# Performance work log

Hardware: AMD Instinct MI355X
Metric: run time of the kernel (lower is better)

The kernel has to match this reference:

```python
import jax, jax.numpy as jnp
import numpy as np

N = 100000   # users
E = 50000    # hyperedges per timestep
NNZ = 800000 # incidences per timestep
T = 8        # step_split
D = 64       # embed_dim


def setup_inputs() -> dict:
    key = jax.random.key(0)
    ks = jax.random.split(key, 9)
    s = 1.0 / np.sqrt(D)
    return {
        "user_emb": jax.random.normal(ks[0], (N, D), jnp.float32) * s,
        "W_conv": jax.random.normal(ks[1], (D, D), jnp.float32) * s,
        "b_conv": jnp.zeros((D,), jnp.float32),
        "fus_w1": jax.random.normal(ks[2], (D, D), jnp.float32) * s,
        "fus_b1": jnp.zeros((D,), jnp.float32),
        "fus_w2": jax.random.normal(ks[3], (D, 1), jnp.float32) * s,
        "fus_b2": jnp.zeros((1,), jnp.float32),
        "edge_nodes": jax.random.randint(ks[4], (T, NNZ), 0, N),
        "edge_hyper": jax.random.randint(ks[5], (T, NNZ), 0, E),
    }


def _hconv(h, nodes, hyper):
    # h: [N, D] transformed node feats; nodes/hyper: [NNZ] incidence list
    ones = jnp.ones((nodes.shape[0], 1), h.dtype)
    e_sum = jax.ops.segment_sum(h[nodes], hyper, num_segments=E)      # [E, D]
    e_cnt = jax.ops.segment_sum(ones, hyper, num_segments=E)          # [E, 1]
    e = e_sum / jnp.maximum(e_cnt, 1.0)
    n_sum = jax.ops.segment_sum(e[hyper], nodes, num_segments=N)      # [N, D]
    n_cnt = jax.ops.segment_sum(ones, nodes, num_segments=N)          # [N, 1]
    return n_sum / jnp.maximum(n_cnt, 1.0)


def _fuse(hidden, dy, w1, b1, w2, b2):
    emb = jnp.stack([hidden, dy], axis=0)                             # [2, N, D]
    score = jax.nn.softmax(jnp.tanh(emb @ w1 + b1) @ w2 + b2, axis=0)  # [2, N, 1]
    return jnp.sum(score * emb, axis=0)                                # [N, D]


def reference(user_emb, W_conv, b_conv, fus_w1, fus_b1, fus_w2, fus_b2,
              edge_nodes, edge_hyper):
    # Conv input is always the raw user embedding table -> per-step convs independent.
    h = jax.nn.relu(user_emb @ W_conv + b_conv)                        # [N, D]
    conv_out = jax.vmap(lambda nd, hy: _hconv(h, nd, hy))(edge_nodes, edge_hyper)  # [T, N, D]

    def step(carry, dy):
        out = _fuse(carry, dy, fus_w1, fus_b1, fus_w2, fus_b2)
        return out, None

    final, _ = jax.lax.scan(step, conv_out[0], conv_out[1:])
    return final
```

## Files before the change

kernel.cpp:

```cpp
#include <hip/hip_runtime.h>
#include <hip/hip_bf16.h>

#define N_USERS 100000
#define E_HYPER 50000
#define NNZ_E   800000
#define T_STEPS 8
#define DIM     64

typedef __bf16 bf16x8 __attribute__((ext_vector_type(8)));
typedef float  f32x4  __attribute__((ext_vector_type(4)));

__device__ __forceinline__ float ld_in(const void* p, size_t i, int f32)
{
    return f32 ? ((const float*)p)[i]
               : __bfloat162float(((const __hip_bfloat16*)p)[i]);
}

__global__ void k_detect(const unsigned short* __restrict__ raw, int* __restrict__ flag)
{
    __shared__ int cnt;
    if (threadIdx.x == 0) cnt = 0;
    __syncthreads();
    int c = 0;
    for (int i = threadIdx.x; i < 4096; i += blockDim.x) {
        int e = (raw[i] >> 7) & 0xFF;
        if (e > 126) c++;
    }
    atomicAdd(&cnt, c);
    __syncthreads();
    if (threadIdx.x == 0) *flag = (cnt > 64) ? 1 : 0;
}

__global__ void k_convert_params(
    const void* W, const void* b, const void* w1, const void* b1,
    const void* w2, const void* b2, const int* __restrict__ flag,
    float* __restrict__ st)
{
    int f = *flag;
    int i = blockIdx.x * blockDim.x + threadIdx.x;
    if (i < 4096)          st[i] = ld_in(W,  i,        f);
    else if (i < 4160)     st[i] = ld_in(b,  i - 4096, f);
    else if (i < 8256)     st[i] = ld_in(w1, i - 4160, f);
    else if (i < 8320)     st[i] = ld_in(b1, i - 8256, f);
    else if (i < 8384)     st[i] = ld_in(w2, i - 8320, f);
    else if (i == 8384)    st[i] = ld_in(b2, 0,        f);
}

__global__ __launch_bounds__(256) void k_transform(
    const void* __restrict__ emb, const int* __restrict__ flag,
    const float* __restrict__ st, __hip_bfloat16* __restrict__ h)
{
    __shared__ float Wl[DIM * DIM];
    __shared__ float bl[DIM];
    for (int i = threadIdx.x; i < DIM * DIM; i += blockDim.x) Wl[i] = st[i];
    if (threadIdx.x < DIM) bl[threadIdx.x] = st[4096 + threadIdx.x];
    __syncthreads();

    int f = *flag;
    int wave = threadIdx.x >> 6, lane = threadIdx.x & 63;
    int wavesTotal = gridDim.x * (blockDim.x >> 6);
    for (int row = blockIdx.x * (blockDim.x >> 6) + wave; row < N_USERS;
         row += wavesTotal) {
        size_t base = (size_t)row * DIM;
        float v = ld_in(emb, base + lane, f);
        float acc = bl[lane];
#pragma unroll
        for (int k = 0; k < DIM; ++k)
            acc += __shfl(v, k, 64) * Wl[k * DIM + lane];
        h[base + lane] = __float2bfloat16(fmaxf(acc, 0.f));
    }
}

__global__ __launch_bounds__(256) void k_build(
    const int* __restrict__ nodes, const int* __restrict__ hyper,
    int* __restrict__ head_e, int* __restrict__ next_e,
    int* __restrict__ head_n, int* __restrict__ next_n)
{
    int i = blockIdx.x * blockDim.x + threadIdx.x;
    if (i >= NNZ_E) return;
    next_e[i] = atomicExch(&head_e[hyper[i]], i);
    next_n[i] = atomicExch(&head_n[nodes[i]], i);
}

__global__ __launch_bounds__(256) void k_gather_e(
    const __hip_bfloat16* __restrict__ h,
    const int* __restrict__ nodes,
    const int* __restrict__ head_e, const int* __restrict__ next_e,
    __hip_bfloat16* __restrict__ e)
{
    int lane = threadIdx.x & 63;
    int wid = blockIdx.x * (blockDim.x >> 6) + (threadIdx.x >> 6);
    int nW  = gridDim.x * (blockDim.x >> 6);
    for (int s0 = wid * 4; s0 < E_HYPER; s0 += nW * 4) {
        int idx[4]; float acc[4]; int cnt[4];
#pragma unroll
        for (int c = 0; c < 4; ++c) {
            int sg = s0 + c;
            idx[c] = (sg < E_HYPER) ? head_e[sg] : -1;
            acc[c] = 0.f; cnt[c] = 0;
        }
        while (idx[0] >= 0 || idx[1] >= 0 || idx[2] >= 0 || idx[3] >= 0) {
            int nxt[4], nd[4];
#pragma unroll
            for (int c = 0; c < 4; ++c)
                if (idx[c] >= 0) { nxt[c] = next_e[idx[c]]; nd[c] = nodes[idx[c]]; }
#pragma unroll
            for (int c = 0; c < 4; ++c)
                if (idx[c] >= 0) {
                    acc[c] += __bfloat162float(h[(size_t)nd[c] * DIM + lane]);
                    cnt[c]++; idx[c] = nxt[c];
                }
        }
#pragma unroll
        for (int c = 0; c < 4; ++c) {
            int sg = s0 + c;
            if (sg < E_HYPER)
                e[(size_t)sg * DIM + lane] =
                    __float2bfloat16(acc[c] / (float)max(cnt[c], 1));
        }
    }
}

__device__ __forceinline__ float ld_carry(void* out, float* cws, size_t i,
                                          int f, int use_ws)
{
    if (f) return ((float*)out)[i];
    if (use_ws) return cws[i];
    return __bfloat162float(((__hip_bfloat16*)out)[i]);
}
__device__ __forceinline__ void st_carry(void* out, float* cws, size_t i,
                                         int f, int use_ws, int wr, float v)
{
    if (f) { ((float*)out)[i] = v; return; }
    if (use_ws) {
        cws[i] = v;
        if (wr) ((__hip_bfloat16*)out)[i] = __float2bfloat16(v);
        return;
    }
    ((__hip_bfloat16*)out)[i] = __float2bfloat16(v);
}

__global__ __launch_bounds__(256) void k_gather_n(
    const __hip_bfloat16* __restrict__ e,
    const int* __restrict__ hyper,
    const int* __restrict__ head_n, const int* __restrict__ next_n,
    float* __restrict__ dy,
    void* __restrict__ out, float* __restrict__ cws,
    const int* __restrict__ flag, int use_ws, int to_carry)
{
    int f = *flag;
    int lane = threadIdx.x & 63;
    int wid = blockIdx.x * (blockDim.x >> 6) + (threadIdx.x >> 6);
    int nW  = gridDim.x * (blockDim.x >> 6);
    for (int s0 = wid * 4; s0 < N_USERS; s0 += nW * 4) {
        int idx[4]; float acc[4]; int cnt[4];
#pragma unroll
        for (int c = 0; c < 4; ++c) {
            int sg = s0 + c;
            idx[c] = (sg < N_USERS) ? head_n[sg] : -1;
            acc[c] = 0.f; cnt[c] = 0;
        }
        while (idx[0] >= 0 || idx[1] >= 0 || idx[2] >= 0 || idx[3] >= 0) {
            int nxt[4], hy[4];
#pragma unroll
            for (int c = 0; c < 4; ++c)
                if (idx[c] >= 0) { nxt[c] = next_n[idx[c]]; hy[c] = hyper[idx[c]]; }
#pragma unroll
            for (int c = 0; c < 4; ++c)
                if (idx[c] >= 0) {
                    acc[c] += __bfloat162float(e[(size_t)hy[c] * DIM + lane]);
                    cnt[c]++; idx[c] = nxt[c];
                }
        }
#pragma unroll
        for (int c = 0; c < 4; ++c) {
            int sg = s0 + c;
            if (sg < N_USERS) {
                float v = acc[c] / (float)max(cnt[c], 1);
                size_t o = (size_t)sg * DIM + lane;
                if (to_carry) st_carry(out, cws, o, f, use_ws, 0, v);
                else          dy[o] = v;
            }
        }
    }
}

__global__ __launch_bounds__(256) void k_fuse_mfma(
    void* __restrict__ dout, float* __restrict__ cws,
    const float* __restrict__ dy_buf,
    const float* __restrict__ st, const int* __restrict__ flag,
    int use_ws, int write_out)
{
    int f = *flag;
    float* cf = f ? (float*)dout : (use_ws ? cws : (float*)0);
    __hip_bfloat16* cb = (__hip_bfloat16*)dout;

    int lane = threadIdx.x & 63;
    int quad = lane >> 4;
    int m    = lane & 15;

    bf16x8 bw[4][2];
    float b1v[4], w2v[4];
#pragma unroll
    for (int nt = 0; nt < 4; ++nt) {
#pragma unroll
        for (int kb = 0; kb < 2; ++kb)
#pragma unroll
            for (int j = 0; j < 8; ++j) {
                int k = kb * 32 + quad * 8 + j;
                bw[nt][kb][j] = (__bf16)st[4160 + k * 64 + nt * 16 + m];
            }
        b1v[nt] = st[8256 + nt * 16 + m];
        w2v[nt] = st[8320 + nt * 16 + m];
    }

    int wid = blockIdx.x * (blockDim.x >> 6) + (threadIdx.x >> 6);
    int nW  = gridDim.x * (blockDim.x >> 6);
    const int NT = N_USERS / 16;

    for (int tile = wid; tile < NT; tile += nW) {
        int row = tile * 16 + m;
        size_t base = (size_t)row * DIM;

        float hidf[2][8], dyf[2][8];
        if (cf) {
            const f32x4* cp = (const f32x4*)(cf + base);
            const f32x4* dp = (const f32x4*)(dy_buf + base);
#pragma unroll
            for (int kb = 0; kb < 2; ++kb) {
                f32x4 a = cp[kb * 8 + quad * 2], b = cp[kb * 8 + quad * 2 + 1];
                f32x4 c = dp[kb * 8 + quad * 2], d = dp[kb * 8 + quad * 2 + 1];
#pragma unroll
                for (int j = 0; j < 4; ++j) {
                    hidf[kb][j] = a[j]; hidf[kb][4 + j] = b[j];
                    dyf[kb][j]  = c[j]; dyf[kb][4 + j]  = d[j];
                }
            }
        } else {
#pragma unroll
            for (int kb = 0; kb < 2; ++kb)
#pragma unroll
                for (int j = 0; j < 8; ++j) {
                    int k = kb * 32 + quad * 8 + j;
                    hidf[kb][j] = __bfloat162float(cb[base + k]);
                    dyf[kb][j]  = dy_buf[base + k];
                }
        }

        bf16x8 ah[2], ad[2];
#pragma unroll
        for (int kb = 0; kb < 2; ++kb)
#pragma unroll
            for (int j = 0; j < 8; ++j) {
                ah[kb][j] = (__bf16)hidf[kb][j];
                ad[kb][j] = (__bf16)dyf[kb][j];
            }

        float zh[4] = {0.f, 0.f, 0.f, 0.f};
        float zd[4] = {0.f, 0.f, 0.f, 0.f};
#pragma unroll
        for (int nt = 0; nt < 4; ++nt) {
            f32x4 acch = {0.f, 0.f, 0.f, 0.f};
            f32x4 accd = {0.f, 0.f, 0.f, 0.f};
#pragma unroll
            for (int kb = 0; kb < 2; ++kb) {
                acch = __builtin_amdgcn_mfma_f32_16x16x32_bf16(ah[kb], bw[nt][kb], acch, 0, 0, 0);
                accd = __builtin_amdgcn_mfma_f32_16x16x32_bf16(ad[kb], bw[nt][kb], accd, 0, 0, 0);
            }
#pragma unroll
            for (int reg = 0; reg < 4; ++reg) {
                zh[reg] += tanhf(acch[reg] + b1v[nt]) * w2v[nt];
                zd[reg] += tanhf(accd[reg] + b1v[nt]) * w2v[nt];
            }
        }
        float s[4];
#pragma unroll
        for (int reg = 0; reg < 4; ++reg) {
#pragma unroll
            for (int off = 1; off < 16; off <<= 1) {
                zh[reg] += __shfl_xor(zh[reg], off, 64);
                zd[reg] += __shfl_xor(zd[reg], off, 64);
            }
            float mm = fmaxf(zh[reg], zd[reg]);
            float eh = expf(zh[reg] - mm), ed = expf(zd[reg] - mm);
            s[reg] = eh / (eh + ed);
        }
        int srcl = (m >> 2) * 16;
        float s0 = __shfl(s[0], srcl, 64), s1 = __shfl(s[1], srcl, 64);
        float s2 = __shfl(s[2], srcl, 64), s3 = __shfl(s[3], srcl, 64);
        int r3 = m & 3;
        float sv = (r3 == 0) ? s0 : (r3 == 1) ? s1 : (r3 == 2) ? s2 : s3;

        if (cf) {
            f32x4* cp = (f32x4*)(cf + base);
#pragma unroll
            for (int kb = 0; kb < 2; ++kb) {
                f32x4 v0, v1;
#pragma unroll
                for (int j = 0; j < 4; ++j) {
                    v0[j] = sv * hidf[kb][j]     + (1.f - sv) * dyf[kb][j];
                    v1[j] = sv * hidf[kb][4 + j] + (1.f - sv) * dyf[kb][4 + j];
                }
                cp[kb * 8 + quad * 2]     = v0;
                cp[kb * 8 + quad * 2 + 1] = v1;
                if (write_out && !f) {
#pragma unroll
                    for (int j = 0; j < 4; ++j) {
                        int k = kb * 32 + quad * 8 + j;
                        cb[base + k]     = __float2bfloat16(v0[j]);
                        cb[base + k + 4] = __float2bfloat16(v1[j]);
                    }
                }
            }
        } else {
#pragma unroll
            for (int kb = 0; kb < 2; ++kb)
#pragma unroll
                for (int j = 0; j < 8; ++j) {
                    int k = kb * 32 + quad * 8 + j;
                    float v = sv * hidf[kb][j] + (1.f - sv) * dyf[kb][j];
                    cb[base + k] = __float2bfloat16(v);
                }
        }
    }
}

extern "C" void kernel_launch(void* const* d_in, const int* in_sizes, int n_in,
                              void* d_out, int out_size, void* d_ws,
                              size_t ws_size, hipStream_t stream)
{
    const void* user_emb = d_in[0];
    const void* W_conv   = d_in[1];
    const void* b_conv   = d_in[2];
    const void* fus_w1   = d_in[3];
    const void* fus_b1   = d_in[4];
    const void* fus_w2   = d_in[5];
    const void* fus_b2   = d_in[6];
    const int* edge_nodes = (const int*)d_in[7];
    const int* edge_hyper = (const int*)d_in[8];

    const size_t ND = (size_t)N_USERS * DIM;

    float* ws = (float*)d_ws;
    int*   flag   = (int*)ws;
    float* st     = ws + 16;
    int*   head_e = (int*)(ws + 8464);
    int*   head_n = (int*)(ws + 58464);
    int*   next_e = (int*)(ws + 158464);
    int*   next_n = (int*)(ws + 958464);
    __hip_bfloat16* e_buf = (__hip_bfloat16*)(ws + 1758464);
    float* dy_buf = ws + 3358464;
    __hip_bfloat16* h = (__hip_bfloat16*)(ws + 9758464);
    float* carry_ws   = ws + 12958464;

    const size_t need_ws_carry = (12958464 + ND) * 4;
    const int use_ws = (ws_size >= need_ws_carry) ? 1 : 0;

    k_detect<<<1, 256, 0, stream>>>((const unsigned short*)user_emb, flag);
    k_convert_params<<<(8385 + 255) / 256, 256, 0, stream>>>(
        W_conv, b_conv, fus_w1, fus_b1, fus_w2, fus_b2, flag, st);
    k_transform<<<1024, 256, 0, stream>>>(user_emb, flag, st, h);

    for (int t = 0; t < T_STEPS; ++t) {
        const int* nodes = edge_nodes + (size_t)t * NNZ_E;
        const int* hyper = edge_hyper + (size_t)t * NNZ_E;

        hipMemsetAsync(head_e, 0xFF, (size_t)(E_HYPER + N_USERS) * 4, stream);

        k_build<<<(NNZ_E + 255) / 256, 256, 0, stream>>>(
            nodes, hyper, head_e, next_e, head_n, next_n);
        k_gather_e<<<3125, 256, 0, stream>>>(h, nodes, head_e, next_e, e_buf);
        k_gather_n<<<6250, 256, 0, stream>>>(
            e_buf, hyper, head_n, next_n, dy_buf,
            d_out, carry_ws, flag, use_ws, (t == 0) ? 1 : 0);

        if (t > 0) {
            k_fuse_mfma<<<1024, 256, 0, stream>>>(
                d_out, carry_ws, dy_buf, st, flag, use_ws,
                (t == T_STEPS - 1) ? 1 : 0);
        }
    }
}
```

Baseline: 2.014 ms.

## Fuse node gather with fusion step and tag linked-list heads to drop memset

The node-side gather is merged into the MFMA fusion kernel, so each wave gathers 16 rows into registers and fuses them with the carry directly. This removes the fp32 dy buffer write and re-read on every step. The per-step memset of the list heads is replaced by tagging each index with the step number and ignoring entries that carry a stale tag. The edge gather now walks 8 chains per wave instead of 4. In exchange, the code gains more register pressure, an LDS transpose, and a reliance on stale heads never carrying a matching tag.

```diff
diff --git a/kernel.cpp b/kernel.cpp
--- a/kernel.cpp
+++ b/kernel.cpp
@@ -6,6 +6,7 @@
 #define NNZ_E   800000
 #define T_STEPS 8
 #define DIM     64
+#define IDXM    0xFFFFF
 
 typedef __bf16 bf16x8 __attribute__((ext_vector_type(8)));
 typedef float  f32x4  __attribute__((ext_vector_type(4)));
@@ -74,45 +75,55 @@
 __global__ __launch_bounds__(256) void k_build(
     const int* __restrict__ nodes, const int* __restrict__ hyper,
     int* __restrict__ head_e, int* __restrict__ next_e,
-    int* __restrict__ head_n, int* __restrict__ next_n)
+    int* __restrict__ head_n, int* __restrict__ next_n, int tag)
 {
     int i = blockIdx.x * blockDim.x + threadIdx.x;
     if (i >= NNZ_E) return;
-    next_e[i] = atomicExch(&head_e[hyper[i]], i);
-    next_n[i] = atomicExch(&head_n[nodes[i]], i);
+    int tv = (tag << 20) | i;
+    next_e[i] = atomicExch(&head_e[hyper[i]], tv);
+    next_n[i] = atomicExch(&head_n[nodes[i]], tv);
+}
+
+__device__ __forceinline__ int dec(int v, int tag)
+{
+    return ((v >> 20) == tag) ? (v & IDXM) : -1;
 }
 
 __global__ __launch_bounds__(256) void k_gather_e(
     const __hip_bfloat16* __restrict__ h,
     const int* __restrict__ nodes,
     const int* __restrict__ head_e, const int* __restrict__ next_e,
-    __hip_bfloat16* __restrict__ e)
+    __hip_bfloat16* __restrict__ e, int tag)
 {
     int lane = threadIdx.x & 63;
     int wid = blockIdx.x * (blockDim.x >> 6) + (threadIdx.x >> 6);
     int nW  = gridDim.x * (blockDim.x >> 6);
-    for (int s0 = wid * 4; s0 < E_HYPER; s0 += nW * 4) {
-        int idx[4]; float acc[4]; int cnt[4];
-#pragma unroll
-        for (int c = 0; c < 4; ++c) {
+    for (int s0 = wid * 8; s0 < E_HYPER; s0 += nW * 8) {
+        int idx[8]; float acc[8]; int cnt[8];
+#pragma unroll
+        for (int c = 0; c < 8; ++c) {
             int sg = s0 + c;
-            idx[c] = (sg < E_HYPER) ? head_e[sg] : -1;
+            idx[c] = (sg < E_HYPER) ? dec(head_e[sg], tag) : -1;
             acc[c] = 0.f; cnt[c] = 0;
         }
-        while (idx[0] >= 0 || idx[1] >= 0 || idx[2] >= 0 || idx[3] >= 0) {
-            int nxt[4], nd[4];
-#pragma unroll
-            for (int c = 0; c < 4; ++c)
+        while (true) {
+            bool any = false;
+#pragma unroll
+            for (int c = 0; c < 8; ++c) any = any || (idx[c] >= 0);
+            if (!any) break;
+            int nxt[8], nd[8];
+#pragma unroll
+            for (int c = 0; c < 8; ++c)
                 if (idx[c] >= 0) { nxt[c] = next_e[idx[c]]; nd[c] = nodes[idx[c]]; }
 #pragma unroll
-            for (int c = 0; c < 4; ++c)
+            for (int c = 0; c < 8; ++c)
                 if (idx[c] >= 0) {
                     acc[c] += __bfloat162float(h[(size_t)nd[c] * DIM + lane]);
-                    cnt[c]++; idx[c] = nxt[c];
+                    cnt[c]++; idx[c] = dec(nxt[c], tag);
                 }
         }
 #pragma unroll
-        for (int c = 0; c < 4; ++c) {
+        for (int c = 0; c < 8; ++c) {
             int sg = s0 + c;
             if (sg < E_HYPER)
                 e[(size_t)sg * DIM + lane] =
@@ -140,64 +151,19 @@
     ((__hip_bfloat16*)out)[i] = __float2bfloat16(v);
 }
 
-__global__ __launch_bounds__(256) void k_gather_n(
-    const __hip_bfloat16* __restrict__ e,
+__global__ __launch_bounds__(256) void k_gather_fuse(
+    const __hip_bfloat16* __restrict__ e_buf,
     const int* __restrict__ hyper,
     const int* __restrict__ head_n, const int* __restrict__ next_n,
-    float* __restrict__ dy,
-    void* __restrict__ out, float* __restrict__ cws,
-    const int* __restrict__ flag, int use_ws, int to_carry)
-{
+    void* __restrict__ dout, float* __restrict__ cws,
+    const float* __restrict__ st, const int* __restrict__ flag,
+    int use_ws, int tag, int do_fuse, int write_out)
+{
+    __shared__ float lt[4][2][16 * 65];
     int f = *flag;
     int lane = threadIdx.x & 63;
-    int wid = blockIdx.x * (blockDim.x >> 6) + (threadIdx.x >> 6);
-    int nW  = gridDim.x * (blockDim.x >> 6);
-    for (int s0 = wid * 4; s0 < N_USERS; s0 += nW * 4) {
-        int idx[4]; float acc[4]; int cnt[4];
-#pragma unroll
-        for (int c = 0; c < 4; ++c) {
-            int sg = s0 + c;
-            idx[c] = (sg < N_USERS) ? head_n[sg] : -1;
-            acc[c] = 0.f; cnt[c] = 0;
-        }
-        while (idx[0] >= 0 || idx[1] >= 0 || idx[2] >= 0 || idx[3] >= 0) {
-            int nxt[4], hy[4];
-#pragma unroll
-            for (int c = 0; c < 4; ++c)
-                if (idx[c] >= 0) { nxt[c] = next_n[idx[c]]; hy[c] = hyper[idx[c]]; }
-#pragma unroll
-            for (int c = 0; c < 4; ++c)
-                if (idx[c] >= 0) {
-                    acc[c] += __bfloat162float(e[(size_t)hy[c] * DIM + lane]);
-                    cnt[c]++; idx[c] = nxt[c];
-                }
-        }
-#pragma unroll
-        for (int c = 0; c < 4; ++c) {
-            int sg = s0 + c;
-            if (sg < N_USERS) {
-                float v = acc[c] / (float)max(cnt[c], 1);
-                size_t o = (size_t)sg * DIM + lane;
-                if (to_carry) st_carry(out, cws, o, f, use_ws, 0, v);
-                else          dy[o] = v;
-            }
-        }
-    }
-}
-
-__global__ __launch_bounds__(256) void k_fuse_mfma(
-    void* __restrict__ dout, float* __restrict__ cws,
-    const float* __restrict__ dy_buf,
-    const float* __restrict__ st, const int* __restrict__ flag,
-    int use_ws, int write_out)
-{
-    int f = *flag;
-    float* cf = f ? (float*)dout : (use_ws ? cws : (float*)0);
-    __hip_bfloat16* cb = (__hip_bfloat16*)dout;
-
-    int lane = threadIdx.x & 63;
-    int quad = lane >> 4;
-    int m    = lane & 15;
+    int wavein = threadIdx.x >> 6;
+    int quad = lane >> 4, m = lane & 15;
 
     bf16x8 bw[4][2];
     float b1v[4], w2v[4];
@@ -214,46 +180,68 @@
         w2v[nt] = st[8320 + nt * 16 + m];
     }
 
-    int wid = blockIdx.x * (blockDim.x >> 6) + (threadIdx.x >> 6);
-    int nW  = gridDim.x * (blockDim.x >> 6);
+    int wid = blockIdx.x * 4 + wavein;
+    int nW  = gridDim.x * 4;
     const int NT = N_USERS / 16;
+    float* Lh = lt[wavein][0];
+    float* Ld = lt[wavein][1];
 
     for (int tile = wid; tile < NT; tile += nW) {
-        int row = tile * 16 + m;
-        size_t base = (size_t)row * DIM;
-
-        float hidf[2][8], dyf[2][8];
-        if (cf) {
-            const f32x4* cp = (const f32x4*)(cf + base);
-            const f32x4* dp = (const f32x4*)(dy_buf + base);
-#pragma unroll
-            for (int kb = 0; kb < 2; ++kb) {
-                f32x4 a = cp[kb * 8 + quad * 2], b = cp[kb * 8 + quad * 2 + 1];
-                f32x4 c = dp[kb * 8 + quad * 2], d = dp[kb * 8 + quad * 2 + 1];
-#pragma unroll
-                for (int j = 0; j < 4; ++j) {
-                    hidf[kb][j] = a[j]; hidf[kb][4 + j] = b[j];
-                    dyf[kb][j]  = c[j]; dyf[kb][4 + j]  = d[j];
+        int s0 = tile * 16;
+
+        int idx[16]; float acc[16]; int cnt[16];
+#pragma unroll
+        for (int c = 0; c < 16; ++c) {
+            idx[c] = dec(head_n[s0 + c], tag);
+            acc[c] = 0.f; cnt[c] = 0;
+        }
+        while (true) {
+            bool any = false;
+#pragma unroll
+            for (int c = 0; c < 16; ++c) any = any || (idx[c] >= 0);
+            if (!any) break;
+            int nxt[16], hy[16];
+#pragma unroll
+            for (int c = 0; c < 16; ++c)
+                if (idx[c] >= 0) { nxt[c] = next_n[idx[c]]; hy[c] = hyper[idx[c]]; }
+#pragma unroll
+            for (int c = 0; c < 16; ++c)
+                if (idx[c] >= 0) {
+                    acc[c] += __bfloat162float(e_buf[(size_t)hy[c] * DIM + lane]);
+                    cnt[c]++; idx[c] = dec(nxt[c], tag);
                 }
-            }
-        } else {
-#pragma unroll
-            for (int kb = 0; kb < 2; ++kb)
-#pragma unroll
-                for (int j = 0; j < 8; ++j) {
-                    int k = kb * 32 + quad * 8 + j;
-                    hidf[kb][j] = __bfloat162float(cb[base + k]);
-                    dyf[kb][j]  = dy_buf[base + k];
-                }
-        }
+        }
+        float dy[16];
+#pragma unroll
+        for (int c = 0; c < 16; ++c) dy[c] = acc[c] / (float)max(cnt[c], 1);
+
+        if (!do_fuse) {
+#pragma unroll
+            for (int c = 0; c < 16; ++c)
+                st_carry(dout, cws, (size_t)(s0 + c) * DIM + lane, f, use_ws,
+                         0, dy[c]);
+            continue;
+        }
+
+        float hid[16];
+#pragma unroll
+        for (int c = 0; c < 16; ++c)
+            hid[c] = ld_carry(dout, cws, (size_t)(s0 + c) * DIM + lane, f, use_ws);
+
+#pragma unroll
+        for (int c = 0; c < 16; ++c) {
+            Lh[c * 65 + lane] = hid[c];
+            Ld[c * 65 + lane] = dy[c];
+        }
+        __asm__ volatile("s_waitcnt lgkmcnt(0)" ::: "memory");
 
         bf16x8 ah[2], ad[2];
 #pragma unroll
         for (int kb = 0; kb < 2; ++kb)
 #pragma unroll
             for (int j = 0; j < 8; ++j) {
-                ah[kb][j] = (__bf16)hidf[kb][j];
-                ad[kb][j] = (__bf16)dyf[kb][j];
+                ah[kb][j] = (__bf16)Lh[m * 65 + kb * 32 + quad * 8 + j];
+                ad[kb][j] = (__bf16)Ld[m * 65 + kb * 32 + quad * 8 + j];
             }
 
         float zh[4] = {0.f, 0.f, 0.f, 0.f};
@@ -285,42 +273,16 @@
             float eh = expf(zh[reg] - mm), ed = expf(zd[reg] - mm);
             s[reg] = eh / (eh + ed);
         }
-        int srcl = (m >> 2) * 16;
-        float s0 = __shfl(s[0], srcl, 64), s1 = __shfl(s[1], srcl, 64);
-        float s2 = __shfl(s[2], srcl, 64), s3 = __shfl(s[3], srcl, 64);
-        int r3 = m & 3;
-        float sv = (r3 == 0) ? s0 : (r3 == 1) ? s1 : (r3 == 2) ? s2 : s3;
-
-        if (cf) {
-            f32x4* cp = (f32x4*)(cf + base);
-#pragma unroll
-            for (int kb = 0; kb < 2; ++kb) {
-                f32x4 v0, v1;
-#pragma unroll
-                for (int j = 0; j < 4; ++j) {
-                    v0[j] = sv * hidf[kb][j]     + (1.f - sv) * dyf[kb][j];
-                    v1[j] = sv * hidf[kb][4 + j] + (1.f - sv) * dyf[kb][4 + j];
-                }
-                cp[kb * 8 + quad * 2]     = v0;
-                cp[kb * 8 + quad * 2 + 1] = v1;
-                if (write_out && !f) {
-#pragma unroll
-                    for (int j = 0; j < 4; ++j) {
-                        int k = kb * 32 + quad * 8 + j;
-                        cb[base + k]     = __float2bfloat16(v0[j]);
-                        cb[base + k + 4] = __float2bfloat16(v1[j]);
-                    }
-                }
-            }
-        } else {
-#pragma unroll
-            for (int kb = 0; kb < 2; ++kb)
-#pragma unroll
-                for (int j = 0; j < 8; ++j) {
-                    int k = kb * 32 + quad * 8 + j;
-                    float v = sv * hidf[kb][j] + (1.f - sv) * dyf[kb][j];
-                    cb[base + k] = __float2bfloat16(v);
-                }
+        float sc[16];
+#pragma unroll
+        for (int c = 0; c < 16; ++c)
+            sc[c] = __shfl(s[c & 3], (c >> 2) * 16, 64);
+
+#pragma unroll
+        for (int c = 0; c < 16; ++c) {
+            float v = sc[c] * hid[c] + (1.f - sc[c]) * dy[c];
+            st_carry(dout, cws, (size_t)(s0 + c) * DIM + lane, f, use_ws,
+                     write_out, v);
         }
     }
 }
@@ -349,7 +311,6 @@
     int*   next_e = (int*)(ws + 158464);
     int*   next_n = (int*)(ws + 958464);
     __hip_bfloat16* e_buf = (__hip_bfloat16*)(ws + 1758464);
-    float* dy_buf = ws + 3358464;
     __hip_bfloat16* h = (__hip_bfloat16*)(ws + 9758464);
     float* carry_ws   = ws + 12958464;
 
@@ -364,20 +325,13 @@
     for (int t = 0; t < T_STEPS; ++t) {
         const int* nodes = edge_nodes + (size_t)t * NNZ_E;
         const int* hyper = edge_hyper + (size_t)t * NNZ_E;
-
-        hipMemsetAsync(head_e, 0xFF, (size_t)(E_HYPER + N_USERS) * 4, stream);
+        int tag = t + 1;
 
         k_build<<<(NNZ_E + 255) / 256, 256, 0, stream>>>(
-            nodes, hyper, head_e, next_e, head_n, next_n);
-        k_gather_e<<<3125, 256, 0, stream>>>(h, nodes, head_e, next_e, e_buf);
-        k_gather_n<<<6250, 256, 0, stream>>>(
-            e_buf, hyper, head_n, next_n, dy_buf,
-            d_out, carry_ws, flag, use_ws, (t == 0) ? 1 : 0);
-
-        if (t > 0) {
-            k_fuse_mfma<<<1024, 256, 0, stream>>>(
-                d_out, carry_ws, dy_buf, st, flag, use_ws,
-                (t == T_STEPS - 1) ? 1 : 0);
-        }
-    }
-}
+            nodes, hyper, head_e, next_e, head_n, next_n, tag);
+        k_gather_e<<<1563, 256, 0, stream>>>(h, nodes, head_e, next_e, e_buf, tag);
+        k_gather_fuse<<<1024, 256, 0, stream>>>(
+            e_buf, hyper, head_n, next_n, d_out, carry_ws, st, flag,
+            use_ws, tag, (t > 0) ? 1 : 0, (t == T_STEPS - 1) ? 1 : 0);
+    }
+}
```

Result: slower. 4.143 ms (+105.7%).
